# Kernel optimization log

Measured on AMD Instinct MI355X. Metric: run time of the kernel, lower is better.

Reference implementation:

```python
import jax, jax.numpy as jnp
import numpy as np

B, S, D = 4, 2048, 1152
H, KVH, HD = 16, 4, 64
SW = 1792
NEG = jnp.float32(-1e9)


def setup_inputs() -> dict:
    key = jax.random.key(0)
    ks = jax.random.split(key, 6)
    x = jax.random.normal(ks[0], (B, S, D), jnp.float32)
    s = 0.02
    wq = jax.random.normal(ks[1], (H * HD, D), jnp.float32) * s
    wk = jax.random.normal(ks[2], (KVH * HD, D), jnp.float32) * s
    wv = jax.random.normal(ks[3], (KVH * HD, D), jnp.float32) * s
    wo = jax.random.normal(ks[4], (D, H * HD), jnp.float32) * s
    # rotary freqs: theta=10000, standard llama-style
    inv = 1.0 / (10000.0 ** (np.arange(0, HD, 2, dtype=np.float32) / HD))
    t = np.arange(S, dtype=np.float32)
    fr = np.outer(t, inv)  # [S, HD//2]
    freqs_cos = jnp.asarray(np.cos(fr), jnp.float32)
    freqs_sin = jnp.asarray(np.sin(fr), jnp.float32)
    positions = jnp.arange(S, dtype=jnp.int32)
    # sliding-window causal additive mask: attend j iff 0 <= i-j < SW
    i = jnp.arange(S)[:, None]
    j = jnp.arange(S)[None, :]
    allowed = (j <= i) & (i - j < SW)
    mask = jnp.where(allowed, jnp.float32(0.0), NEG)
    cache_k = jnp.zeros((B, SW, KVH, HD), jnp.float32)
    cache_v = jnp.zeros((B, SW, KVH, HD), jnp.float32)
    return {"x": x, "wq": wq, "wk": wk, "wv": wv, "wo": wo,
            "freqs_cos": freqs_cos, "freqs_sin": freqs_sin, "mask": mask,
            "cache_k": cache_k, "cache_v": cache_v, "positions": positions}


def _rope(t, cos, sin):
    # t: [B,S,h,HD]; complex multiply on (even, odd) pairs
    tr = t.reshape(t.shape[:-1] + (HD // 2, 2))
    a, b = tr[..., 0], tr[..., 1]
    c = cos[None, :, None, :]
    s = sin[None, :, None, :]
    out = jnp.stack([a * c - b * s, a * s + b * c], axis=-1)
    return out.reshape(t.shape)


def reference(x, wq, wk, wv, wo, freqs_cos, freqs_sin, mask, cache_k, cache_v, positions):
    bsz, seqlen, _ = x.shape
    xq = jnp.einsum('bsd,ed->bse', x, wq).reshape(bsz, seqlen, H, HD)
    xk = jnp.einsum('bsd,ed->bse', x, wk).reshape(bsz, seqlen, KVH, HD)
    xv = jnp.einsum('bsd,ed->bse', x, wv).reshape(bsz, seqlen, KVH, HD)
    xq = _rope(xq, freqs_cos, freqs_sin)
    xk = _rope(xk, freqs_cos, freqs_sin)
    # circular-buffer cache scatter (last SW tokens, modulo indexing)
    idx = positions[-SW:] % SW
    new_ck = cache_k.at[:, idx].set(xk[:, -SW:])
    new_cv = cache_v.at[:, idx].set(xv[:, -SW:])
    # GQA: expand kv heads (repeat_interleave on head dim)
    rep = H // KVH
    key = jnp.repeat(xk, rep, axis=2)   # [B,S,H,HD]
    value = jnp.repeat(xv, rep, axis=2)
    q = xq.transpose(0, 2, 1, 3)        # [B,H,S,HD]
    k = key.transpose(0, 2, 1, 3)
    v = value.transpose(0, 2, 1, 3)
    scale = 1.0 / jnp.sqrt(jnp.float32(HD))
    scores = jnp.einsum('bhqd,bhkd->bhqk', q, k) * scale + mask[None, None]
    probs = jax.nn.softmax(scores, axis=-1)
    out = jnp.einsum('bhqk,bhkd->bhqd', probs, v)
    out = out.transpose(0, 2, 1, 3).reshape(bsz, seqlen, H * HD)
    out = jnp.einsum('bse,de->bsd', out, wo)
    return out, new_ck, new_cv
```

## Files before the change

### kernel.cpp

```cpp
#include <hip/hip_runtime.h>
#include <cstdint>
#include <cstddef>


typedef unsigned short u16;
typedef unsigned int   u32;
typedef __attribute__((ext_vector_type(8))) short bf16x8;
typedef __attribute__((ext_vector_type(4))) float f32x4;

#define AS1(p) ((const __attribute__((address_space(1))) void*)(p))
#define AS3(p) ((__attribute__((address_space(3))) void*)(p))

__device__ __forceinline__ u16 f2bf(float f) {
  u32 u = __float_as_uint(f);
  u += 0x7fffu + ((u >> 16) & 1u);
  return (u16)(u >> 16);
}
__device__ __forceinline__ float bf2f(u32 x) { return __uint_as_float(x << 16); }
__device__ __forceinline__ f32x4 mfma16(bf16x8 a, bf16x8 b, f32x4 c) {
  return __builtin_amdgcn_mfma_f32_16x16x32_bf16(a, b, c, 0, 0, 0);
}
__device__ __forceinline__ u32 cvtpk_bf16(float lo, float hi) {
  u32 r;
  asm("v_cvt_pk_bf16_f32 %0, %1, %2" : "=v"(r) : "v"(lo), "v"(hi));
  return r;
}

__global__ __launch_bounds__(256) void cvt_kernel(const float* __restrict__ in,
                                                  u16* __restrict__ out, int n4) {
  int i = blockIdx.x * 256 + threadIdx.x;
  if (i >= n4) return;
  float4 v = ((const float4*)in)[i];
  uint2 o;
  o.x = (u32)f2bf(v.x) | ((u32)f2bf(v.y) << 16);
  o.y = (u32)f2bf(v.z) | ((u32)f2bf(v.w) << 16);
  ((uint2*)out)[i] = o;
}

template<int BF16_OUT>
__global__ __launch_bounds__(256) void gemm_bt(const u16* __restrict__ A,
                                               const u16* __restrict__ B,
                                               void* __restrict__ C,
                                               int M, int N, int K) {
  __shared__ u16 As[128][64];
  __shared__ u16 Bs[128][64];
  const int tid  = threadIdx.x;
  const int w    = tid >> 6, lane = tid & 63;
  const int l15  = lane & 15, hi4 = lane >> 4;
  const int m0   = blockIdx.y * 128, n0 = blockIdx.x * 128;
  const int wr   = w >> 1, wc = w & 1;

  const int srow = lane >> 3;
  const int scol = ((lane & 7) ^ srow) << 3;
  const u16* Ab = A + (size_t)(m0 + w * 32 + srow) * K + scol;
  const u16* Bb = B + (size_t)(n0 + w * 32 + srow) * K + scol;
  u16* AsDst = &As[w * 32][0];
  u16* BsDst = &Bs[w * 32][0];

  const int swz = (l15 & 7) << 4;
  const int c0  = (((hi4 * 16)      ^ swz) >> 1);
  const int c1  = (((64 + hi4 * 16) ^ swz) >> 1);
  const u16* aRd = &As[wr * 64 + l15][0];
  const u16* bRd = &Bs[wc * 64 + l15][0];

  f32x4 acc[4][4] = {};

  for (int kk = 0; kk < K; kk += 64) {
#pragma unroll
    for (int q = 0; q < 4; q++) {
      __builtin_amdgcn_global_load_lds(AS1(Ab + kk + (size_t)q * 8 * K),
                                       AS3(AsDst + q * 8 * 64), 16, 0, 0);
      __builtin_amdgcn_global_load_lds(AS1(Bb + kk + (size_t)q * 8 * K),
                                       AS3(BsDst + q * 8 * 64), 16, 0, 0);
    }
    __syncthreads();
#pragma unroll
    for (int ks = 0; ks < 2; ks++) {
      const int cc = ks ? c1 : c0;
      bf16x8 af[4], bfr[4];
#pragma unroll
      for (int t = 0; t < 4; t++) af[t]  = *(const bf16x8*)(aRd + t * 16 * 64 + cc);
#pragma unroll
      for (int t = 0; t < 4; t++) bfr[t] = *(const bf16x8*)(bRd + t * 16 * 64 + cc);
#pragma unroll
      for (int mi = 0; mi < 4; mi++)
#pragma unroll
        for (int ni = 0; ni < 4; ni++)
          acc[mi][ni] = mfma16(af[mi], bfr[ni], acc[mi][ni]);
    }
    __syncthreads();
  }

#pragma unroll
  for (int mi = 0; mi < 4; mi++) {
#pragma unroll
    for (int r = 0; r < 4; r++) {
      int row = m0 + wr * 64 + mi * 16 + hi4 * 4 + r;
      size_t base = (size_t)row * N + n0 + wc * 64 + l15;
#pragma unroll
      for (int ni = 0; ni < 4; ni++) {
        float v = acc[mi][ni][r];
        if (BF16_OUT) ((u16*)C)[base + ni * 16] = f2bf(v);
        else          ((float*)C)[base + ni * 16] = v;
      }
    }
  }
}

template<int PAIRS, int COLOFF, bool QSCALE>
__global__ __launch_bounds__(256) void rope_kernel(u16* __restrict__ buf,
                                                   float* __restrict__ cache,
                                                   const float* __restrict__ cosT,
                                                   const float* __restrict__ sinT) {
  int idx = blockIdx.x * 256 + threadIdx.x;
  int m = idx / PAIRS, p = idx % PAIRS;
  int s = m & 2047, b = m >> 11;
  int hh = p & 31;
  u32* bp = (u32*)buf + (size_t)m * 768 + COLOFF + p;
  u32 pk = *bp;
  float a  = bf2f(pk & 0xffffu), bb = bf2f(pk >> 16);
  float c  = cosT[s * 32 + hh],  sn = sinT[s * 32 + hh];
  float o0 = a * c - bb * sn;
  float o1 = a * sn + bb * c;
  const float qs = QSCALE ? 0.18033688011112042f : 1.0f;
  *bp = (u32)f2bf(o0 * qs) | ((u32)f2bf(o1 * qs) << 16);
  if (!QSCALE && s >= 256) {
    int pc = (s < 1792) ? s : s - 1792;
    float2* cp = (float2*)(cache + (size_t)(b * 1792 + pc) * 256 + 2 * p);
    *cp = make_float2(o0, o1);
  }
}

__global__ __launch_bounds__(256) void vfuse_kernel(const u16* __restrict__ qkv,
                                                    u16* __restrict__ vT,
                                                    float* __restrict__ ncv) {
  __shared__ u16 tile[64][65];
  int s0 = blockIdx.x * 64, kvh = blockIdx.y, b = blockIdx.z;
  int t = threadIdx.x;
  int r = t >> 2, cc = (t & 3) * 16;
  const u16* src = qkv + (size_t)(b * 2048 + s0 + r) * 1536 + 1280 + kvh * 64 + cc;
  uint4 v0 = *(const uint4*)src;
  uint4 v1 = *(const uint4*)(src + 8);
  u16 vals[16];
  *(uint4*)&vals[0] = v0;
  *(uint4*)&vals[8] = v1;
  int s = s0 + r;
  if (s >= 256) {
    int pc = (s < 1792) ? s : s - 1792;
    float* dst = ncv + (size_t)(b * 1792 + pc) * 256 + kvh * 64 + cc;
#pragma unroll
    for (int i = 0; i < 16; i += 4) {
      float4 f = make_float4(bf2f(vals[i]), bf2f(vals[i + 1]),
                             bf2f(vals[i + 2]), bf2f(vals[i + 3]));
      *(float4*)(dst + i) = f;
    }
  }
#pragma unroll
  for (int i = 0; i < 16; i++) tile[cc + i][r] = vals[i];
  __syncthreads();
  u16 ov[16];
#pragma unroll
  for (int i = 0; i < 16; i++) ov[i] = tile[r][cc + i];
  u16* dst2 = vT + (size_t)((b * 4 + kvh) * 64 + r) * 2048 + s0 + cc;
  *(uint4*)dst2 = *(uint4*)&ov[0];
  *(uint4*)(dst2 + 8) = *(uint4*)&ov[8];
}

__global__ __launch_bounds__(256) void attn_kernel(const u16* __restrict__ qkv,
                                                   const u16* __restrict__ vT,
                                                   u16* __restrict__ attnb) {
  __shared__ __align__(16) u16 Kbuf[4][32][64];
  __shared__ __align__(16) u16 Vbuf[4][64][32];
  __shared__ __align__(16) u16 P[4][2][16][40];
  const int tid = threadIdx.x;
  const int w = tid >> 6, lane = tid & 63;
  const int l15 = lane & 15, hi4 = lane >> 4;
  const int gx = blockIdx.x;
  const int kvh = blockIdx.y, b = blockIdx.z;
  const int h = kvh * 4 + w;

  const int nseg = (gx < 28) ? 2 : 1;
  const int cA = (gx < 28) ? (55 - gx) : (gx + 28);

  const u16* qbase = qkv + (size_t)(b * 2048) * 1536 + h * 64;
  const u16* kbase = qkv + (size_t)(b * 2048) * 1536 + 1024 + kvh * 64;
  const u16* vbase = vT + (size_t)((b * 4 + kvh) * 64) * 2048;

  const int kr  = 8 * w + (lane >> 3);
  const int ksl = (lane & 7) ^ (lane >> 3);
  const int vr  = 16 * w + (lane >> 2);
  const int vsl = (lane & 3) ^ ((lane >> 2) & 3);

  bf16x8 ones;
#pragma unroll
  for (int i = 0; i < 8; i++) ones[i] = (short)0x3F80;

#define STAGE(J0, BS)                                                                    \
  do {                                                                                   \
    __builtin_amdgcn_global_load_lds(AS1(kbase + (size_t)((J0) + kr) * 1536 + ksl * 8),  \
                                     AS3(&Kbuf[BS][8 * w][0]), 16, 0, 0);                \
    __builtin_amdgcn_global_load_lds(AS1(vbase + (size_t)vr * 2048 + (J0) + vsl * 8),    \
                                     AS3(&Vbuf[BS][16 * w][0]), 16, 0, 0);               \
  } while (0)

  for (int sg = 0; sg < nseg; sg++) {
    const int i0 = 32 * (sg == 0 ? cA : gx);
    __syncthreads();

    bf16x8 qa[2][2];
    {
      const u16* qp = qbase + (size_t)(i0 + l15) * 1536 + hi4 * 8;
#pragma unroll
      for (int m = 0; m < 2; m++)
#pragma unroll
        for (int kf_i = 0; kf_i < 2; kf_i++)
          qa[m][kf_i] = *(const bf16x8*)(qp + m * 16 * 1536 + kf_i * 32);
    }

    f32x4 o[2][4] = {};
    f32x4 ol[2] = {};

    int jstart = i0 - 1791;
    if (jstart < 0) jstart = 0;
    jstart &= ~31;
    const int jend = i0 + 32;

    STAGE(jstart, 0);
    if (jstart + 32 < jend) STAGE(jstart + 32, 1);

    int it = 0;
    for (int j0 = jstart; j0 < jend; j0 += 32, it++) {
      if (j0 + 64 < jend) {
        STAGE(j0 + 64, (it + 2) & 3);
        asm volatile("s_waitcnt vmcnt(4)" ::: "memory");
      } else if (j0 + 32 < jend) {
        asm volatile("s_waitcnt vmcnt(2)" ::: "memory");
      } else {
        asm volatile("s_waitcnt vmcnt(0)" ::: "memory");
      }
      __builtin_amdgcn_s_barrier();
      __builtin_amdgcn_sched_barrier(0);

      const u16* Kb = &Kbuf[it & 3][0][0];
      const u16* Vb = &Vbuf[it & 3][0][0];
      bf16x8 kf[2][2], vf[4];
#pragma unroll
      for (int kf_i = 0; kf_i < 2; kf_i++)
#pragma unroll
        for (int nt = 0; nt < 2; nt++) {
          int s = nt * 16 + l15;
          int ph = (kf_i * 4 + hi4) ^ (l15 & 7);
          kf[kf_i][nt] = *(const bf16x8*)(Kb + s * 64 + ph * 8);
        }
#pragma unroll
      for (int t = 0; t < 4; t++) {
        int rv = 16 * t + l15;
        int pv = hi4 ^ (l15 & 3);
        vf[t] = *(const bf16x8*)(Vb + rv * 32 + pv * 8);
      }

      f32x4 sc[2][2] = {};
#pragma unroll
      for (int m = 0; m < 2; m++)
#pragma unroll
        for (int nt = 0; nt < 2; nt++) {
          sc[m][nt] = mfma16(kf[0][nt], qa[m][0], sc[m][nt]);
          sc[m][nt] = mfma16(kf[1][nt], qa[m][1], sc[m][nt]);
        }

      float p[2][2][4];
      const bool fast = (j0 + 31 <= i0) && (i0 + 31 - j0 < 1792);
      if (fast) {
#pragma unroll
        for (int m = 0; m < 2; m++)
#pragma unroll
          for (int nt = 0; nt < 2; nt++)
#pragma unroll
            for (int r = 0; r < 4; r++)
              p[m][nt][r] = __builtin_amdgcn_exp2f(sc[m][nt][r]);
      } else {
#pragma unroll
        for (int m = 0; m < 2; m++)
#pragma unroll
          for (int nt = 0; nt < 2; nt++) {
#pragma unroll
            for (int r = 0; r < 4; r++) {
              const int i = i0 + m * 16 + l15;
              const int j = j0 + nt * 16 + hi4 * 4 + r;
              p[m][nt][r] = (j <= i && i - j < 1792)
                              ? __builtin_amdgcn_exp2f(sc[m][nt][r]) : 0.f;
            }
          }
      }

#pragma unroll
      for (int m = 0; m < 2; m++)
#pragma unroll
        for (int nt = 0; nt < 2; nt++) {
          uint2 pk;
          pk.x = cvtpk_bf16(p[m][nt][0], p[m][nt][1]);
          pk.y = cvtpk_bf16(p[m][nt][2], p[m][nt][3]);
          *(uint2*)&P[w][m][l15][nt * 16 + hi4 * 4] = pk;
        }
      asm volatile("s_waitcnt lgkmcnt(0)" ::: "memory");
      __builtin_amdgcn_sched_barrier(0);

      bf16x8 pa[2];
#pragma unroll
      for (int m = 0; m < 2; m++)
        pa[m] = *(const bf16x8*)&P[w][m][l15][hi4 * 8];

#pragma unroll
      for (int m = 0; m < 2; m++) {
#pragma unroll
        for (int t = 0; t < 4; t++) o[m][t] = mfma16(pa[m], vf[t], o[m][t]);
        ol[m] = mfma16(pa[m], ones, ol[m]);
      }
    }

    u16* op = attnb + (size_t)(b * 2048 + i0 + hi4 * 4) * 1024 + h * 64 + l15;
#pragma unroll
    for (int m = 0; m < 2; m++)
#pragma unroll
      for (int r = 0; r < 4; r++) {
        float inv = 1.0f / ol[m][r];
#pragma unroll
        for (int t = 0; t < 4; t++)
          op[(size_t)(m * 16 + r) * 1024 + 16 * t] = f2bf(o[m][t][r] * inv);
      }
  }
#undef STAGE
}

extern "C" void kernel_launch(void* const* d_in, const int* in_sizes, int n_in,
                              void* d_out, int out_size, void* d_ws, size_t ws_size,
                              hipStream_t stream) {
  const float* x  = (const float*)d_in[0];
  const float* wq = (const float*)d_in[1];
  const float* wk = (const float*)d_in[2];
  const float* wv = (const float*)d_in[3];
  const float* wo = (const float*)d_in[4];
  const float* fc = (const float*)d_in[5];
  const float* fs = (const float*)d_in[6];

  float* out = (float*)d_out;
  float* nck = out + 9437184;
  float* ncv = nck + 1835008;

  char* ws = (char*)d_ws;
  u16* xb    = (u16*)(ws);
  u16* wqkvb = (u16*)(ws + 18874368);
  u16* wob   = (u16*)(ws + 22413312);
  u16* qkv   = (u16*)(ws + 24772608);
  u16* vT    = (u16*)(ws + 49938432);
  u16* attnb = (u16*)(ws + 54132736);

  cvt_kernel<<<9216, 256, 0, stream>>>(x,  xb, 2359296);
  cvt_kernel<<<1152, 256, 0, stream>>>(wq, wqkvb, 294912);
  cvt_kernel<<<288,  256, 0, stream>>>(wk, wqkvb + 1024 * 1152, 73728);
  cvt_kernel<<<288,  256, 0, stream>>>(wv, wqkvb + 1280 * 1152, 73728);
  cvt_kernel<<<1152, 256, 0, stream>>>(wo, wob, 294912);

  gemm_bt<1><<<dim3(12, 64), 256, 0, stream>>>(xb, wqkvb, qkv, 8192, 1536, 1152);

  rope_kernel<512, 0,   true ><<<16384, 256, 0, stream>>>(qkv, nullptr, fc, fs);
  rope_kernel<128, 512, false><<<4096,  256, 0, stream>>>(qkv, nck, fc, fs);

  vfuse_kernel<<<dim3(32, 4, 4), 256, 0, stream>>>(qkv, vT, ncv);

  attn_kernel<<<dim3(36, 4, 4), 256, 0, stream>>>(qkv, vT, attnb);

  gemm_bt<0><<<dim3(9, 64), 256, 0, stream>>>(attnb, wob, out, 8192, 1152, 1024);
}
```

Measured before the change: 182.8 us.

## Merge conversion launches and restructure attention into 64-key tiles with one query block per workgroup

The five fp32-to-bf16 conversion launches become one kernel that picks its source buffer from the thread index, removing per-launch overhead. The attention kernel now handles a single 32-row query block per workgroup (1024 workgroups, remapped across XCDs, heaviest blocks first) instead of pairing blocks, and processes 64 keys per iteration with a double-buffered LDS ring instead of 32 keys with a quad buffer. It also raises wave priority around the MFMA section and issues the next prefetch after a second barrier. The larger tiles halve loop and barrier overhead per key, but the extra barrier and the shallower prefetch depth may expose more memory latency, and load balance now relies on the grid ordering.

```diff
diff --git a/kernel.cpp b/kernel.cpp
--- a/kernel.cpp
+++ b/kernel.cpp
@@ -26,15 +26,26 @@
   return r;
 }
 
-__global__ __launch_bounds__(256) void cvt_kernel(const float* __restrict__ in,
-                                                  u16* __restrict__ out, int n4) {
+__global__ __launch_bounds__(256) void cvt5_kernel(const float* __restrict__ x,
+                                                   const float* __restrict__ wq,
+                                                   const float* __restrict__ wk,
+                                                   const float* __restrict__ wv,
+                                                   const float* __restrict__ wo,
+                                                   u16* __restrict__ xb,
+                                                   u16* __restrict__ wqkvb,
+                                                   u16* __restrict__ wob) {
   int i = blockIdx.x * 256 + threadIdx.x;
-  if (i >= n4) return;
-  float4 v = ((const float4*)in)[i];
+  const float* in; u16* out; int off;
+  if (i < 2359296)      { in = x;  out = xb;                  off = i; }
+  else if (i < 2654208) { in = wq; out = wqkvb;               off = i - 2359296; }
+  else if (i < 2727936) { in = wk; out = wqkvb + 1024 * 1152; off = i - 2654208; }
+  else if (i < 2801664) { in = wv; out = wqkvb + 1280 * 1152; off = i - 2727936; }
+  else                  { in = wo; out = wob;                 off = i - 2801664; }
+  float4 v = ((const float4*)in)[off];
   uint2 o;
   o.x = (u32)f2bf(v.x) | ((u32)f2bf(v.y) << 16);
   o.y = (u32)f2bf(v.z) | ((u32)f2bf(v.w) << 16);
-  ((uint2*)out)[i] = o;
+  ((uint2*)out)[off] = o;
 }
 
 template<int BF16_OUT>
@@ -169,167 +180,147 @@
 __global__ __launch_bounds__(256) void attn_kernel(const u16* __restrict__ qkv,
                                                    const u16* __restrict__ vT,
                                                    u16* __restrict__ attnb) {
-  __shared__ __align__(16) u16 Kbuf[4][32][64];
-  __shared__ __align__(16) u16 Vbuf[4][64][32];
-  __shared__ __align__(16) u16 P[4][2][16][40];
+  __shared__ __align__(16) u16 Kbuf[2][64][64];
+  __shared__ __align__(16) u16 Vbuf[2][64][64];
+  __shared__ __align__(16) u16 P[4][16][72];
   const int tid = threadIdx.x;
   const int w = tid >> 6, lane = tid & 63;
   const int l15 = lane & 15, hi4 = lane >> 4;
-  const int gx = blockIdx.x;
-  const int kvh = blockIdx.y, b = blockIdx.z;
-  const int h = kvh * 4 + w;
-
-  const int nseg = (gx < 28) ? 2 : 1;
-  const int cA = (gx < 28) ? (55 - gx) : (gx + 28);
+
+  const int lid  = blockIdx.x + 64 * (blockIdx.y + 4 * blockIdx.z);
+  const int wgid = (lid & 7) * 128 + (lid >> 3);
+  const int gx   = wgid & 63;
+  const int rr   = wgid >> 6;
+  const int kvh  = rr & 3, b = rr >> 2;
+  const int i0   = 32 * (63 - gx);
+  const int h    = kvh * 4 + w;
 
   const u16* qbase = qkv + (size_t)(b * 2048) * 1536 + h * 64;
   const u16* kbase = qkv + (size_t)(b * 2048) * 1536 + 1024 + kvh * 64;
   const u16* vbase = vT + (size_t)((b * 4 + kvh) * 64) * 2048;
 
-  const int kr  = 8 * w + (lane >> 3);
-  const int ksl = (lane & 7) ^ (lane >> 3);
-  const int vr  = 16 * w + (lane >> 2);
-  const int vsl = (lane & 3) ^ ((lane >> 2) & 3);
+  bf16x8 qa[2][2];
+  {
+    const u16* qp = qbase + (size_t)(i0 + l15) * 1536 + hi4 * 8;
+#pragma unroll
+    for (int m = 0; m < 2; m++)
+#pragma unroll
+      for (int ki = 0; ki < 2; ki++)
+        qa[m][ki] = *(const bf16x8*)(qp + m * 16 * 1536 + ki * 32);
+  }
 
   bf16x8 ones;
 #pragma unroll
   for (int i = 0; i < 8; i++) ones[i] = (short)0x3F80;
 
-#define STAGE(J0, BS)                                                                    \
-  do {                                                                                   \
-    __builtin_amdgcn_global_load_lds(AS1(kbase + (size_t)((J0) + kr) * 1536 + ksl * 8),  \
-                                     AS3(&Kbuf[BS][8 * w][0]), 16, 0, 0);                \
-    __builtin_amdgcn_global_load_lds(AS1(vbase + (size_t)vr * 2048 + (J0) + vsl * 8),    \
-                                     AS3(&Vbuf[BS][16 * w][0]), 16, 0, 0);               \
+  f32x4 o[2][4] = {};
+  f32x4 ol[2] = {};
+
+  const int srow = lane >> 3;
+  const int ssl  = (lane & 7) ^ srow;
+
+#define STAGE(J0, BS)                                                                     \
+  do {                                                                                    \
+    _Pragma("unroll")                                                                     \
+    for (int q = 0; q < 2; q++) {                                                         \
+      const int row = 32 * q + 8 * w + srow;                                              \
+      __builtin_amdgcn_global_load_lds(AS1(kbase + (size_t)((J0) + row) * 1536 + ssl * 8),\
+                                       AS3(&Kbuf[BS][32 * q + 8 * w][0]), 16, 0, 0);      \
+      __builtin_amdgcn_global_load_lds(AS1(vbase + (size_t)row * 2048 + (J0) + ssl * 8),  \
+                                       AS3(&Vbuf[BS][32 * q + 8 * w][0]), 16, 0, 0);      \
+    }                                                                                     \
   } while (0)
 
-  for (int sg = 0; sg < nseg; sg++) {
-    const int i0 = 32 * (sg == 0 ? cA : gx);
-    __syncthreads();
-
-    bf16x8 qa[2][2];
-    {
-      const u16* qp = qbase + (size_t)(i0 + l15) * 1536 + hi4 * 8;
-#pragma unroll
-      for (int m = 0; m < 2; m++)
-#pragma unroll
-        for (int kf_i = 0; kf_i < 2; kf_i++)
-          qa[m][kf_i] = *(const bf16x8*)(qp + m * 16 * 1536 + kf_i * 32);
-    }
-
-    f32x4 o[2][4] = {};
-    f32x4 ol[2] = {};
-
-    int jstart = i0 - 1791;
-    if (jstart < 0) jstart = 0;
-    jstart &= ~31;
-    const int jend = i0 + 32;
-
-    STAGE(jstart, 0);
-    if (jstart + 32 < jend) STAGE(jstart + 32, 1);
-
-    int it = 0;
-    for (int j0 = jstart; j0 < jend; j0 += 32, it++) {
-      if (j0 + 64 < jend) {
-        STAGE(j0 + 64, (it + 2) & 3);
-        asm volatile("s_waitcnt vmcnt(4)" ::: "memory");
-      } else if (j0 + 32 < jend) {
-        asm volatile("s_waitcnt vmcnt(2)" ::: "memory");
-      } else {
-        asm volatile("s_waitcnt vmcnt(0)" ::: "memory");
+  int jstart = i0 - 1791;
+  if (jstart < 0) jstart = 0;
+  jstart &= ~63;
+  const int jend = i0 + 32;
+  const int ntiles = (jend - jstart + 63) >> 6;
+
+  STAGE(jstart, 0);
+  if (ntiles > 1) STAGE(jstart + 64, 1);
+
+  for (int t = 0; t < ntiles; t++) {
+    const int j0 = jstart + 64 * t;
+    if (t + 1 < ntiles) asm volatile("s_waitcnt vmcnt(4)" ::: "memory");
+    else                asm volatile("s_waitcnt vmcnt(0)" ::: "memory");
+    __builtin_amdgcn_s_barrier();
+    __builtin_amdgcn_sched_barrier(0);
+
+    const u16* Kb = &Kbuf[t & 1][0][0];
+    const u16* Vb = &Vbuf[t & 1][0][0];
+    bf16x8 kf[2][4], vf[4][2];
+#pragma unroll
+    for (int nt = 0; nt < 4; nt++)
+#pragma unroll
+      for (int ki = 0; ki < 2; ki++)
+        kf[ki][nt] = *(const bf16x8*)(Kb + (nt * 16 + l15) * 64 +
+                                      (((ki * 4 + hi4) ^ (l15 & 7)) << 3));
+#pragma unroll
+    for (int tt = 0; tt < 4; tt++)
+#pragma unroll
+      for (int kc = 0; kc < 2; kc++)
+        vf[tt][kc] = *(const bf16x8*)(Vb + (tt * 16 + l15) * 64 +
+                                      (((kc * 4 + hi4) ^ (l15 & 7)) << 3));
+    asm volatile("s_waitcnt lgkmcnt(0)" ::: "memory");
+    __builtin_amdgcn_sched_barrier(0);
+    __builtin_amdgcn_s_barrier();
+    if (t + 2 < ntiles) STAGE(j0 + 128, t & 1);
+
+    __builtin_amdgcn_s_setprio(1);
+    const bool fast = (j0 + 63 <= i0) && (i0 + 31 - j0 < 1792);
+#pragma unroll
+    for (int m = 0; m < 2; m++) {
+      uint2 pk[4];
+#pragma unroll
+      for (int nt = 0; nt < 4; nt++) {
+        f32x4 s = {0.f, 0.f, 0.f, 0.f};
+        s = mfma16(kf[0][nt], qa[m][0], s);
+        s = mfma16(kf[1][nt], qa[m][1], s);
+        float p[4];
+        if (fast) {
+#pragma unroll
+          for (int r = 0; r < 4; r++) p[r] = __builtin_amdgcn_exp2f(s[r]);
+        } else {
+#pragma unroll
+          for (int r = 0; r < 4; r++) {
+            const int j = j0 + nt * 16 + hi4 * 4 + r;
+            const int i = i0 + m * 16 + l15;
+            p[r] = (j <= i && i - j < 1792) ? __builtin_amdgcn_exp2f(s[r]) : 0.f;
+          }
+        }
+        pk[nt].x = cvtpk_bf16(p[0], p[1]);
+        pk[nt].y = cvtpk_bf16(p[2], p[3]);
       }
-      __builtin_amdgcn_s_barrier();
-      __builtin_amdgcn_sched_barrier(0);
-
-      const u16* Kb = &Kbuf[it & 3][0][0];
-      const u16* Vb = &Vbuf[it & 3][0][0];
-      bf16x8 kf[2][2], vf[4];
-#pragma unroll
-      for (int kf_i = 0; kf_i < 2; kf_i++)
-#pragma unroll
-        for (int nt = 0; nt < 2; nt++) {
-          int s = nt * 16 + l15;
-          int ph = (kf_i * 4 + hi4) ^ (l15 & 7);
-          kf[kf_i][nt] = *(const bf16x8*)(Kb + s * 64 + ph * 8);
-        }
-#pragma unroll
-      for (int t = 0; t < 4; t++) {
-        int rv = 16 * t + l15;
-        int pv = hi4 ^ (l15 & 3);
-        vf[t] = *(const bf16x8*)(Vb + rv * 32 + pv * 8);
-      }
-
-      f32x4 sc[2][2] = {};
-#pragma unroll
-      for (int m = 0; m < 2; m++)
-#pragma unroll
-        for (int nt = 0; nt < 2; nt++) {
-          sc[m][nt] = mfma16(kf[0][nt], qa[m][0], sc[m][nt]);
-          sc[m][nt] = mfma16(kf[1][nt], qa[m][1], sc[m][nt]);
-        }
-
-      float p[2][2][4];
-      const bool fast = (j0 + 31 <= i0) && (i0 + 31 - j0 < 1792);
-      if (fast) {
-#pragma unroll
-        for (int m = 0; m < 2; m++)
-#pragma unroll
-          for (int nt = 0; nt < 2; nt++)
-#pragma unroll
-            for (int r = 0; r < 4; r++)
-              p[m][nt][r] = __builtin_amdgcn_exp2f(sc[m][nt][r]);
-      } else {
-#pragma unroll
-        for (int m = 0; m < 2; m++)
-#pragma unroll
-          for (int nt = 0; nt < 2; nt++) {
-#pragma unroll
-            for (int r = 0; r < 4; r++) {
-              const int i = i0 + m * 16 + l15;
-              const int j = j0 + nt * 16 + hi4 * 4 + r;
-              p[m][nt][r] = (j <= i && i - j < 1792)
-                              ? __builtin_amdgcn_exp2f(sc[m][nt][r]) : 0.f;
-            }
-          }
-      }
-
-#pragma unroll
-      for (int m = 0; m < 2; m++)
-#pragma unroll
-        for (int nt = 0; nt < 2; nt++) {
-          uint2 pk;
-          pk.x = cvtpk_bf16(p[m][nt][0], p[m][nt][1]);
-          pk.y = cvtpk_bf16(p[m][nt][2], p[m][nt][3]);
-          *(uint2*)&P[w][m][l15][nt * 16 + hi4 * 4] = pk;
-        }
+#pragma unroll
+      for (int nt = 0; nt < 4; nt++)
+        *(uint2*)&P[w][l15][nt * 16 + hi4 * 4] = pk[nt];
       asm volatile("s_waitcnt lgkmcnt(0)" ::: "memory");
       __builtin_amdgcn_sched_barrier(0);
-
-      bf16x8 pa[2];
-#pragma unroll
-      for (int m = 0; m < 2; m++)
-        pa[m] = *(const bf16x8*)&P[w][m][l15][hi4 * 8];
-
-#pragma unroll
-      for (int m = 0; m < 2; m++) {
-#pragma unroll
-        for (int t = 0; t < 4; t++) o[m][t] = mfma16(pa[m], vf[t], o[m][t]);
-        ol[m] = mfma16(pa[m], ones, ol[m]);
+      bf16x8 pa0 = *(const bf16x8*)&P[w][l15][hi4 * 8];
+      bf16x8 pa1 = *(const bf16x8*)&P[w][l15][32 + hi4 * 8];
+#pragma unroll
+      for (int tt = 0; tt < 4; tt++) {
+        o[m][tt] = mfma16(pa0, vf[tt][0], o[m][tt]);
+        o[m][tt] = mfma16(pa1, vf[tt][1], o[m][tt]);
       }
-    }
-
-    u16* op = attnb + (size_t)(b * 2048 + i0 + hi4 * 4) * 1024 + h * 64 + l15;
-#pragma unroll
-    for (int m = 0; m < 2; m++)
-#pragma unroll
-      for (int r = 0; r < 4; r++) {
-        float inv = 1.0f / ol[m][r];
-#pragma unroll
-        for (int t = 0; t < 4; t++)
-          op[(size_t)(m * 16 + r) * 1024 + 16 * t] = f2bf(o[m][t][r] * inv);
-      }
+      ol[m] = mfma16(pa0, ones, ol[m]);
+      ol[m] = mfma16(pa1, ones, ol[m]);
+    }
+    __builtin_amdgcn_s_setprio(0);
   }
 #undef STAGE
+
+  u16* op = attnb + (size_t)(b * 2048 + i0 + hi4 * 4) * 1024 + h * 64 + l15;
+#pragma unroll
+  for (int m = 0; m < 2; m++)
+#pragma unroll
+    for (int r = 0; r < 4; r++) {
+      float inv = 1.0f / ol[m][r];
+#pragma unroll
+      for (int tt = 0; tt < 4; tt++)
+        op[(size_t)(m * 16 + r) * 1024 + 16 * tt] = f2bf(o[m][tt][r] * inv);
+    }
 }
 
 extern "C" void kernel_launch(void* const* d_in, const int* in_sizes, int n_in,
@@ -355,11 +346,7 @@
   u16* vT    = (u16*)(ws + 49938432);
   u16* attnb = (u16*)(ws + 54132736);
 
-  cvt_kernel<<<9216, 256, 0, stream>>>(x,  xb, 2359296);
-  cvt_kernel<<<1152, 256, 0, stream>>>(wq, wqkvb, 294912);
-  cvt_kernel<<<288,  256, 0, stream>>>(wk, wqkvb + 1024 * 1152, 73728);
-  cvt_kernel<<<288,  256, 0, stream>>>(wv, wqkvb + 1280 * 1152, 73728);
-  cvt_kernel<<<1152, 256, 0, stream>>>(wo, wob, 294912);
+  cvt5_kernel<<<12096, 256, 0, stream>>>(x, wq, wk, wv, wo, xb, wqkvb, wob);
 
   gemm_bt<1><<<dim3(12, 64), 256, 0, stream>>>(xb, wqkvb, qkv, 8192, 1536, 1152);
 
@@ -368,7 +355,7 @@
 
   vfuse_kernel<<<dim3(32, 4, 4), 256, 0, stream>>>(qkv, vT, ncv);
 
-  attn_kernel<<<dim3(36, 4, 4), 256, 0, stream>>>(qkv, vT, attnb);
+  attn_kernel<<<dim3(64, 4, 4), 256, 0, stream>>>(qkv, vT, attnb);
 
   gemm_bt<0><<<dim3(9, 64), 256, 0, stream>>>(attnb, wob, out, 8192, 1152, 1024);
 }
```

New measurement: 167.7 us. -8.3%, faster.
